# Optimization experiments

Hardware: AMD Instinct MI355X
Metric: run time of the kernel (lower is better)

Reference implementation:

```python
import jax, jax.numpy as jnp
import numpy as np

B, T, D = 2, 1024, 1024
H, HKV = 16, 8
HD = D // H           # 64
NREP = H // HKV       # 2
NLAYERS = 3
MAXKV = T * NLAYERS   # 3072
EPS = 1e-5


def setup_inputs() -> dict:
    key = jax.random.key(0)
    ks = jax.random.split(key, 8)
    # rotary tables over full accumulated-KV range
    inv_freq = 1.0 / (10000.0 ** (jnp.arange(0, HD, 2, dtype=jnp.float32) / HD))  # (HD/2,)
    t = jnp.arange(MAXKV, dtype=jnp.float32)
    freqs = jnp.outer(t, inv_freq)  # (MAXKV, HD/2)
    return {
        "x": jax.random.normal(ks[0], (B, T, D), jnp.float32),
        "cos": jnp.cos(freqs),
        "sin": jnp.sin(freqs),
        "q_w": jax.random.normal(ks[1], (NLAYERS, D, D), jnp.float32) * 0.02,
        "k_w": jax.random.normal(ks[2], (NLAYERS, D // NREP, D), jnp.float32) * 0.02,
        "v_w": jax.random.normal(ks[3], (NLAYERS, D // NREP, D), jnp.float32) * 0.02,
        "ln_w": jnp.ones((NLAYERS, D), jnp.float32),
        "lam": jax.random.normal(ks[4], (NLAYERS,), jnp.float32) * 0.1,
        "out_w": jax.random.normal(ks[5], (D, D), jnp.float32) * 0.02,
        "final_ln_w": jnp.ones((D,), jnp.float32),
        "alpha": jnp.ones((1,), jnp.float32),
    }


def rmsnorm(x, w):
    return x * jax.lax.rsqrt(jnp.mean(x * x, axis=-1, keepdims=True) + EPS) * w


def rope(x, cos, sin):
    # x: (B, L, h, HD); cos/sin: (MAXKV, HD/2); flash_attn non-interleaved rotary
    L = x.shape[1]
    c = jnp.concatenate([cos[:L], cos[:L]], axis=-1)[None, :, None, :]
    s = jnp.concatenate([sin[:L], sin[:L]], axis=-1)[None, :, None, :]
    x1, x2 = jnp.split(x, 2, axis=-1)
    rot = jnp.concatenate([-x2, x1], axis=-1)
    return x * c + rot * s


def reference(x, cos, sin, q_w, k_w, v_w, ln_w, lam, out_w, final_ln_w, alpha):
    scale = HD ** -0.5
    # lambda weights: layernorm over sigmoid of the 3 scalars (biased var, eps=1e-5)
    s = jax.nn.sigmoid(lam)
    lw = (s - s.mean()) * jax.lax.rsqrt(s.var() + EPS)
    qidx = jnp.arange(T)
    k_list, v_list = [], []
    acc = jnp.zeros_like(x)
    for i in range(NLAYERS):
        q = (x @ q_w[i].T).reshape(B, T, H, HD)
        k = (x @ k_w[i].T).reshape(B, T, HKV, HD)
        v = (x @ v_w[i].T).reshape(B, T, HKV, HD)
        k_list.append(k)
        v_list.append(v)
        K = jnp.concatenate(k_list, axis=1)  # (B, L, HKV, HD), L=(i+1)*T
        V = jnp.concatenate(v_list, axis=1)
        L = K.shape[1]
        qr = rope(q, cos, sin)
        Kr = rope(K, cos, sin)  # whole buffer re-rotated each layer, as in original
        Kr = jnp.repeat(Kr, NREP, axis=2)  # GQA expand
        Vr = jnp.repeat(V, NREP, axis=2)
        scores = jnp.einsum('bqhd,bkhd->bhqk', qr, Kr) * scale
        # flash_attn causal=True with kv_len > q_len aligns bottom-right
        mask = jnp.arange(L)[None, :] <= (qidx + (L - T))[:, None]
        scores = jnp.where(mask[None, None], scores, -jnp.inf)
        attn = jax.nn.softmax(scores, axis=-1)
        o = jnp.einsum('bhqk,bkhd->bqhd', attn, Vr).reshape(B, T, D)
        acc = acc + rmsnorm(o, ln_w[i]) * lw[i]
    out = rmsnorm(acc + alpha * x, final_ln_w)
    return out @ out_w.T
```

## Files before the change

kernel.cpp:

```cpp
#include <hip/hip_runtime.h>
#include <type_traits>
#include <utility>

typedef unsigned short u16;
typedef unsigned int u32;
typedef short short8 __attribute__((ext_vector_type(8)));
typedef __bf16 bf16x8 __attribute__((ext_vector_type(8)));
typedef float floatx4 __attribute__((ext_vector_type(4)));

template <typename V, typename = void> struct MfmaTakes : std::false_type {};
template <typename V>
struct MfmaTakes<V, std::void_t<decltype(__builtin_amdgcn_mfma_f32_16x16x32_bf16(
    std::declval<V>(), std::declval<V>(), std::declval<floatx4>(), 0, 0, 0))>>
    : std::true_type {};

template <typename V>
__device__ __forceinline__ floatx4 mfma_impl(V a, V b, floatx4 c, std::true_type) {
  return __builtin_amdgcn_mfma_f32_16x16x32_bf16(a, b, c, 0, 0, 0);
}
template <typename V>
__device__ __forceinline__ floatx4 mfma_impl(V a, V b, floatx4 c, std::false_type) {
  return __builtin_amdgcn_mfma_f32_16x16x32_bf16(
      __builtin_bit_cast(bf16x8, a), __builtin_bit_cast(bf16x8, b), c, 0, 0, 0);
}
__device__ __forceinline__ floatx4 MFMA16(short8 a, short8 b, floatx4 c) {
  return mfma_impl<short8>(a, b, c, MfmaTakes<short8>{});
}

__device__ __forceinline__ u16 f2bf(float f) {
  union { float f; unsigned u; } x; x.f = f;
  unsigned r = (x.u + 0x7fffu + ((x.u >> 16) & 1u)) >> 16;
  return (u16)r;
}
__device__ __forceinline__ float bf2f(u16 v) {
  union { unsigned u; float f; } x; x.u = ((unsigned)v) << 16; return x.f;
}
__device__ __forceinline__ u32 packbf(float lo, float hi) {
  return (__float_as_uint(hi) & 0xffff0000u) | (__float_as_uint(lo) >> 16);
}
__device__ __forceinline__ u32 pack2bf(float lo, float hi) {
  return ((u32)f2bf(hi) << 16) | (u32)f2bf(lo);
}

#if defined(__has_builtin)
#if __has_builtin(__builtin_amdgcn_global_load_lds)
#define HAS_GLLDS 1
#endif
#endif
__device__ __forceinline__ void stage16(const u16* g, u16* lbase, int lane) {
#ifdef HAS_GLLDS
  __builtin_amdgcn_global_load_lds(
      (__attribute__((address_space(1))) void*)(g),
      (__attribute__((address_space(3))) void*)(lbase), 16, 0, 0);
#else
  *(uint4*)(lbase + lane * 8) = *(const uint4*)g;
#endif
}

__global__ __launch_bounds__(256) void prep_kernel(
    const float* __restrict__ x, const float* __restrict__ qw,
    const float* __restrict__ kw, const float* __restrict__ vw,
    const float* __restrict__ outw, const float* __restrict__ lam,
    u16* __restrict__ xb, u16* __restrict__ wcat, u16* __restrict__ outwb,
    float* __restrict__ lwbuf) {
  size_t gid = (size_t)blockIdx.x * 256 + threadIdx.x;
  if (gid == 0) {
    float s0 = 1.f / (1.f + expf(-lam[0]));
    float s1 = 1.f / (1.f + expf(-lam[1]));
    float s2 = 1.f / (1.f + expf(-lam[2]));
    float mean = (s0 + s1 + s2) * (1.f / 3.f);
    float d0 = s0 - mean, d1 = s1 - mean, d2 = s2 - mean;
    float var = (d0 * d0 + d1 * d1 + d2 * d2) * (1.f / 3.f);
    float r = rsqrtf(var + 1e-5f);
    lwbuf[0] = d0 * r; lwbuf[1] = d1 * r; lwbuf[2] = d2 * r;
  }
  if (gid < 524288) {
    float4 v = ((const float4*)x)[gid];
    ushort4 o; o.x = f2bf(v.x); o.y = f2bf(v.y); o.z = f2bf(v.z); o.w = f2bf(v.w);
    ((ushort4*)xb)[gid] = o;
    return;
  }
  size_t g2 = gid - 524288;
  if (g2 < 1572864) {
    int col4 = (int)(g2 & 255);
    int n = (int)(g2 >> 8);
    int layer = n >> 11, r = n & 2047;
    const float* srcrow;
    if (r < 1024) srcrow = qw + ((size_t)(layer * 1024 + r) << 10);
    else if (r < 1536) srcrow = kw + ((size_t)(layer * 512 + (r - 1024)) << 10);
    else srcrow = vw + ((size_t)(layer * 512 + (r - 1536)) << 10);
    float4 v = ((const float4*)srcrow)[col4];
    ushort4 o; o.x = f2bf(v.x); o.y = f2bf(v.y); o.z = f2bf(v.z); o.w = f2bf(v.w);
    ((ushort4*)wcat)[g2] = o;
    return;
  }
  size_t g3 = g2 - 1572864;
  if (g3 < 262144) {
    float4 v = ((const float4*)outw)[g3];
    ushort4 o; o.x = f2bf(v.x); o.y = f2bf(v.y); o.z = f2bf(v.z); o.w = f2bf(v.w);
    ((ushort4*)outwb)[g3] = o;
  }
}

__global__ __launch_bounds__(256) void gemm_qkv(
    const u16* __restrict__ A, const u16* __restrict__ Bw,
    const float* __restrict__ cosb, const float* __restrict__ sinb,
    u16* __restrict__ qr, u16* __restrict__ kr, u16* __restrict__ vt) {
  __shared__ u16 As[128][64];
  __shared__ u16 Bs[128][64];
  const unsigned flat = blockIdx.x;
  const int bm = (flat >> 3) & 15;
  const int bn = ((flat >> 7) << 3) + (flat & 7);
  const int tid = threadIdx.x;
  const int wave = tid >> 6, lane = tid & 63;
  const int quad = lane >> 4, l16 = lane & 15;
  const int wm = wave & 1, wn = wave >> 1;
  const int srow = lane >> 3, skc = (lane & 7) * 8;
  floatx4 acc[4][4];
#pragma unroll
  for (int i = 0; i < 4; i++)
#pragma unroll
    for (int j = 0; j < 4; j++) { acc[i][j][0] = 0.f; acc[i][j][1] = 0.f; acc[i][j][2] = 0.f; acc[i][j][3] = 0.f; }
  const u16* Abase = A + (size_t)(bm * 128) * 1024;
  const u16* Bbase = Bw + (size_t)(bn * 128) * 1024;
  for (int k0 = 0; k0 < 1024; k0 += 64) {
    __syncthreads();
#pragma unroll
    for (int i = 0; i < 4; i++) {
      int ch = wave * 4 + i;
      stage16(Abase + (size_t)(ch * 8 + srow) * 1024 + k0 + skc, &As[ch * 8][0], lane);
      stage16(Bbase + (size_t)(ch * 8 + srow) * 1024 + k0 + skc, &Bs[ch * 8][0], lane);
    }
    __syncthreads();
#pragma unroll
    for (int kf = 0; kf < 2; kf++) {
      short8 af[4], bf[4];
#pragma unroll
      for (int mi = 0; mi < 4; mi++)
        af[mi] = *(const short8*)(&As[wm * 64 + mi * 16 + l16][kf * 32 + quad * 8]);
#pragma unroll
      for (int ni = 0; ni < 4; ni++)
        bf[ni] = *(const short8*)(&Bs[wn * 64 + ni * 16 + l16][kf * 32 + quad * 8]);
#pragma unroll
      for (int mi = 0; mi < 4; mi++)
#pragma unroll
        for (int ni = 0; ni < 4; ni++)
          acc[mi][ni] = MFMA16(af[mi], bf[ni], acc[mi][ni]);
    }
  }
  __syncthreads();
  u16* Tw = (&As[0][0]) + (unsigned)wave * 1056;
  const int f0 = bn * 128 + wn * 64;
  const int lay = f0 >> 11;
  const int r0 = f0 & 2047;
  const int mrow0 = bm * 128 + wm * 64;
  const int jrd = lane & 7, trd = lane >> 3;
  if (r0 < 1536) {
    const bool isQ = (r0 < 1024);
    const int h = isQ ? (r0 >> 6) : ((r0 - 1024) >> 6);
    const float qscale = isQ ? 0.125f : 1.f;
    const int posoff = isQ ? 0 : lay * 1024;
#pragma unroll
    for (int mi = 0; mi < 4; mi++) {
#pragma unroll
      for (int rr = 0; rr < 4; rr++) {
        int m = mrow0 + mi * 16 + quad * 4 + rr;
        int t = m & 1023;
        int pos = posoff + t;
        const float* cp = cosb + (size_t)pos * 32;
        const float* sp = sinb + (size_t)pos * 32;
        float c0 = cp[l16], s0 = sp[l16];
        float c1 = cp[16 + l16], s1 = sp[16 + l16];
        float x10 = acc[mi][0][rr], x20 = acc[mi][2][rr];
        float x11 = acc[mi][1][rr], x21 = acc[mi][3][rr];
        u16* trow = Tw + (quad * 4 + rr) * 66;
        trow[l16]      = f2bf((x10 * c0 - x20 * s0) * qscale);
        trow[16 + l16] = f2bf((x11 * c1 - x21 * s1) * qscale);
        trow[32 + l16] = f2bf((x20 * c0 + x10 * s0) * qscale);
        trow[48 + l16] = f2bf((x21 * c1 + x11 * s1) * qscale);
      }
#pragma unroll
      for (int half = 0; half < 2; half++) {
        int tloc = trd + half * 8;
        uint4 val = *(const uint4*)(Tw + tloc * 66 + jrd * 8);
        int m = mrow0 + mi * 16 + tloc;
        int b = m >> 10, t = m & 1023;
        u16* dst;
        if (isQ) dst = qr + ((((size_t)lay * 2 + b) * 16 + h) * 1024 + t) * 64;
        else     dst = kr + (((size_t)(b * 8 + h)) * 3072 + lay * 1024 + t) * 64;
        *(uint4*)(dst + jrd * 8) = val;
      }
    }
  } else {
    const int hv = (r0 - 1536) >> 6;
    const int b = mrow0 >> 10;
    const int posb = lay * 1024 + (mrow0 & 1023);
#pragma unroll
    for (int ni = 0; ni < 4; ni++) {
#pragma unroll
      for (int mi = 0; mi < 4; mi++) {
        u16* trow = Tw + l16 * 66 + mi * 16 + quad * 4;
        trow[0] = f2bf(acc[mi][ni][0]);
        trow[1] = f2bf(acc[mi][ni][1]);
        trow[2] = f2bf(acc[mi][ni][2]);
        trow[3] = f2bf(acc[mi][ni][3]);
      }
#pragma unroll
      for (int half = 0; half < 2; half++) {
        int dloc = trd + half * 8;
        uint4 val = *(const uint4*)(Tw + dloc * 66 + jrd * 8);
        u16* dst = vt + ((size_t)(b * 8 + hv) * 64 + ni * 16 + dloc) * 3072 + posb + jrd * 8;
        *(uint4*)dst = val;
      }
    }
  }
}

__global__ __launch_bounds__(256) void gemm_bt(
    const u16* __restrict__ A, const u16* __restrict__ Bw,
    float* __restrict__ C, int N, int K) {
  __shared__ u16 As[64][72];
  __shared__ u16 Bs[64][72];
  const int bm = blockIdx.x, bn = blockIdx.y;
  const int tid = threadIdx.x;
  const int wave = tid >> 6, lane = tid & 63;
  const int quad = lane >> 4, l16 = lane & 15;
  const int lr = tid >> 2, lc = (tid & 3) << 4;
  floatx4 acc[4];
#pragma unroll
  for (int i = 0; i < 4; i++) { acc[i][0] = 0.f; acc[i][1] = 0.f; acc[i][2] = 0.f; acc[i][3] = 0.f; }
  const u16* Arow = A + (size_t)(bm * 64 + lr) * K;
  const u16* Brow = Bw + (size_t)(bn * 64 + lr) * K;
  for (int k0 = 0; k0 < K; k0 += 64) {
    __syncthreads();
    *(uint4*)(&As[lr][lc])     = *(const uint4*)(Arow + k0 + lc);
    *(uint4*)(&As[lr][lc + 8]) = *(const uint4*)(Arow + k0 + lc + 8);
    *(uint4*)(&Bs[lr][lc])     = *(const uint4*)(Brow + k0 + lc);
    *(uint4*)(&Bs[lr][lc + 8]) = *(const uint4*)(Brow + k0 + lc + 8);
    __syncthreads();
    const int mrow = wave * 16 + l16;
    short8 a0 = *(const short8*)(&As[mrow][quad * 8]);
    short8 a1 = *(const short8*)(&As[mrow][32 + quad * 8]);
#pragma unroll
    for (int ns = 0; ns < 4; ns++) {
      short8 b0 = *(const short8*)(&Bs[ns * 16 + l16][quad * 8]);
      short8 b1 = *(const short8*)(&Bs[ns * 16 + l16][32 + quad * 8]);
      acc[ns] = MFMA16(a0, b0, acc[ns]);
      acc[ns] = MFMA16(a1, b1, acc[ns]);
    }
  }
#pragma unroll
  for (int ns = 0; ns < 4; ns++)
#pragma unroll
    for (int r = 0; r < 4; r++) {
      int row = bm * 64 + wave * 16 + quad * 4 + r;
      int col = bn * 64 + ns * 16 + l16;
      C[(size_t)row * N + col] = acc[ns][r];
    }
}

__global__ __launch_bounds__(256) void attn_v7(
    const u16* __restrict__ qr, const u16* __restrict__ kr,
    const u16* __restrict__ vt, u16* __restrict__ obS,
    float* __restrict__ lbufp) {
  __shared__ u16 Kt2[2][32][40];
  __shared__ u16 Vtt[64][40];
  const unsigned flat = blockIdx.x;
  const int bhz = (int)((flat & 7) + ((flat >> 5) << 3));
  const int qtile = 3 - (int)((flat >> 3) & 3);
  const int z = bhz >> 5;
  const int bh = bhz & 31;
  const int lay = (z == 5) ? 0 : ((z == 0 || z == 4) ? 1 : 2);
  const int n = lay * 32 + qtile * 8 + 8;
  int kt0, kt1;
  if (lay == 0) { kt0 = 0; kt1 = n; }
  else if (lay == 1) { int hf = n >> 1; kt0 = (z == 0) ? 0 : hf; kt1 = (z == 0) ? hf : n; }
  else {
    int t1 = n / 3, t2 = (2 * n) / 3;
    kt0 = (z == 1) ? 0 : ((z == 2) ? t1 : t2);
    kt1 = (z == 1) ? t1 : ((z == 2) ? t2 : n);
  }
  const int maskkt = lay * 32 + qtile * 8;
  const int b = bh >> 4, h = bh & 15, hk = h >> 1;
  const int tid = threadIdx.x, wave = tid >> 6, lane = tid & 63;
  const int quad = lane >> 4, l16 = lane & 15;
  const int qeffbase = lay * 1024 + qtile * 256 + wave * 64;
  const u16* qpb = qr + ((((size_t)lay * 2 + b) * 16 + h) * 1024
                         + qtile * 256 + wave * 64 + l16) * 64 + quad * 8;
  short8 qf[4][2];
#pragma unroll
  for (int nt = 0; nt < 4; nt++) {
    qf[nt][0] = *(const short8*)(qpb + nt * 1024);
    qf[nt][1] = *(const short8*)(qpb + nt * 1024 + 32);
  }
  const short8 ones = {16256, 16256, 16256, 16256, 16256, 16256, 16256, 16256};
  floatx4 oacc[4][4];
#pragma unroll
  for (int nt = 0; nt < 4; nt++)
#pragma unroll
    for (int dt = 0; dt < 4; dt++) { oacc[nt][dt][0] = 0.f; oacc[nt][dt][1] = 0.f; oacc[nt][dt][2] = 0.f; oacc[nt][dt][3] = 0.f; }
  floatx4 lacc[4];
#pragma unroll
  for (int nt = 0; nt < 4; nt++) { lacc[nt][0] = 0.f; lacc[nt][1] = 0.f; lacc[nt][2] = 0.f; lacc[nt][3] = 0.f; }
  const int ksr = tid >> 3, ksc = (tid & 7) * 8;
  const int ksl = ((ksr >> 3) << 2) + (ksr & 3) + (((ksr >> 2) & 1) << 4);
  u16* kdst = (ksc < 32) ? &Kt2[0][ksl][ksc] : &Kt2[1][ksl][ksc - 32];
  const int vdr = tid >> 2, vdc = (tid & 3) * 8;
  const u16* kp = kr + ((size_t)(b * 8 + hk) * 3072 + kt0 * 32 + ksr) * 64 + ksc;
  const u16* vp = vt + ((size_t)(b * 8 + hk) * 64 + vdr) * 3072 + kt0 * 32 + vdc;
  uint4 kA = *(const uint4*)kp;
  uint4 vA = *(const uint4*)vp;
  for (int kt = kt0; kt < kt1; kt++) {
    kp += 2048; vp += 32;
    __syncthreads();
    *(uint4*)kdst = kA;
    *(uint4*)(&Vtt[vdr][vdc]) = vA;
    if (kt + 1 < kt1) { kA = *(const uint4*)kp; vA = *(const uint4*)vp; }
    __syncthreads();
    const bool needmask = (kt >= maskkt);
    uint2 pk[4][2];
#pragma unroll
    for (int mt = 0; mt < 2; mt++) {
      short8 kfa = *(const short8*)(&Kt2[0][mt * 16 + l16][quad * 8]);
      short8 kfb = *(const short8*)(&Kt2[1][mt * 16 + l16][quad * 8]);
      const int keyb = kt * 32 + quad * 8 + mt * 4;
#pragma unroll
      for (int nt = 0; nt < 4; nt++) {
        floatx4 s; s[0] = 0.f; s[1] = 0.f; s[2] = 0.f; s[3] = 0.f;
        s = MFMA16(kfa, qf[nt][0], s);
        s = MFMA16(kfb, qf[nt][1], s);
        float p0 = __expf(s[0]), p1 = __expf(s[1]);
        float p2 = __expf(s[2]), p3 = __expf(s[3]);
        if (needmask) {
          int qpos = qeffbase + nt * 16 + l16;
          if (keyb + 0 > qpos) p0 = 0.f;
          if (keyb + 1 > qpos) p1 = 0.f;
          if (keyb + 2 > qpos) p2 = 0.f;
          if (keyb + 3 > qpos) p3 = 0.f;
        }
        pk[nt][mt].x = packbf(p0, p1);
        pk[nt][mt].y = packbf(p2, p3);
      }
    }
    short8 vf[4];
#pragma unroll
    for (int dt = 0; dt < 4; dt++)
      vf[dt] = *(const short8*)(&Vtt[dt * 16 + l16][quad * 8]);
#pragma unroll
    for (int nt = 0; nt < 4; nt++) {
      union { uint4 u; short8 s; } pf;
      pf.u.x = pk[nt][0].x; pf.u.y = pk[nt][0].y;
      pf.u.z = pk[nt][1].x; pf.u.w = pk[nt][1].y;
      lacc[nt] = MFMA16(ones, pf.s, lacc[nt]);
#pragma unroll
      for (int dt = 0; dt < 4; dt++)
        oacc[nt][dt] = MFMA16(vf[dt], pf.s, oacc[nt][dt]);
    }
  }
  __syncthreads();
  float* Pf = (float*)(&Kt2[0][0][0]) + (unsigned)wave * 320;
  const int tt = lane >> 2, dd = (lane & 3) << 2;
#pragma unroll
  for (int nt = 0; nt < 4; nt++) {
    int t = qtile * 256 + wave * 64 + nt * 16 + l16;
    if (quad == 0)
      lbufp[((size_t)z * 2048 + b * 1024 + t) * 16 + h] = lacc[nt][0];
    int t2 = qtile * 256 + wave * 64 + nt * 16 + tt;
    u16* orow = obS + ((size_t)(z * 2 + b) * 1024 + t2) * 1024 + h * 64 + dd;
#pragma unroll
    for (int dt = 0; dt < 4; dt++) {
      *(floatx4*)(&Pf[l16 * 20 + quad * 4]) = oacc[nt][dt];
      floatx4 val = *(const floatx4*)(&Pf[tt * 20 + dd]);
      uint2 st; st.x = pack2bf(val[0], val[1]); st.y = pack2bf(val[2], val[3]);
      *(uint2*)(orow + dt * 16) = st;
    }
  }
}

__device__ __forceinline__ float block_sum(float v, float* red) {
  v += __shfl_xor(v, 32); v += __shfl_xor(v, 16); v += __shfl_xor(v, 8);
  v += __shfl_xor(v, 4);  v += __shfl_xor(v, 2);  v += __shfl_xor(v, 1);
  __syncthreads();
  if ((threadIdx.x & 63) == 0) red[threadIdx.x >> 6] = v;
  __syncthreads();
  return red[0] + red[1] + red[2] + red[3];
}

__global__ __launch_bounds__(256) void fused_norm(
    const u16* __restrict__ obS, const float* __restrict__ lbufp,
    const float* __restrict__ x, const float* __restrict__ lnw,
    const float* __restrict__ lwbuf, const float* __restrict__ flnw,
    const float* __restrict__ alphap, u16* __restrict__ y) {
  __shared__ float red[4];
  const int row = blockIdx.x, tid = threadIdx.x;
  float a[4] = {0.f, 0.f, 0.f, 0.f};
  const int nsl[3] = {1, 2, 3};
  const int sl[3][3] = {{5, 0, 0}, {0, 4, 0}, {1, 2, 3}};
#pragma unroll
  for (int l = 0; l < 3; l++) {
    float o0 = 0.f, o1 = 0.f, o2 = 0.f, o3 = 0.f, ls = 0.f;
#pragma unroll
    for (int si = 0; si < 3; si++) {
      if (si >= nsl[l]) break;
      int z = sl[l][si];
      uint2 v = ((const uint2*)(obS + ((size_t)z * 2048 + row) * 1024))[tid];
      o0 += bf2f((u16)(v.x & 0xffff)); o1 += bf2f((u16)(v.x >> 16));
      o2 += bf2f((u16)(v.y & 0xffff)); o3 += bf2f((u16)(v.y >> 16));
      ls += lbufp[((size_t)z * 2048 + row) * 16 + (tid >> 4)];
    }
    float linv = 1.f / ls;
    float v0 = o0 * linv, v1 = o1 * linv, v2 = o2 * linv, v3 = o3 * linv;
    float ss = v0 * v0 + v1 * v1 + v2 * v2 + v3 * v3;
    ss = block_sum(ss, red);
    float rstd = rsqrtf(ss * (1.f / 1024.f) + 1e-5f);
    float lw = lwbuf[l];
    float4 w = ((const float4*)(lnw + (size_t)l * 1024))[tid];
    a[0] += v0 * rstd * w.x * lw;
    a[1] += v1 * rstd * w.y * lw;
    a[2] += v2 * rstd * w.z * lw;
    a[3] += v3 * rstd * w.w * lw;
  }
  const float aa = alphap[0];
  float4 xv = ((const float4*)(x + (size_t)row * 1024))[tid];
  float v0 = a[0] + aa * xv.x, v1 = a[1] + aa * xv.y;
  float v2 = a[2] + aa * xv.z, v3 = a[3] + aa * xv.w;
  float ss = v0 * v0 + v1 * v1 + v2 * v2 + v3 * v3;
  ss = block_sum(ss, red);
  float rstd = rsqrtf(ss * (1.f / 1024.f) + 1e-5f);
  float4 fw = ((const float4*)flnw)[tid];
  ushort4 o;
  o.x = f2bf(v0 * rstd * fw.x); o.y = f2bf(v1 * rstd * fw.y);
  o.z = f2bf(v2 * rstd * fw.z); o.w = f2bf(v3 * rstd * fw.w);
  ((ushort4*)(y + (size_t)row * 1024))[tid] = o;
}

extern "C" void kernel_launch(void* const* d_in, const int* in_sizes, int n_in,
                              void* d_out, int out_size, void* d_ws, size_t ws_size,
                              hipStream_t stream) {
  const float* x     = (const float*)d_in[0];
  const float* cosb  = (const float*)d_in[1];
  const float* sinb  = (const float*)d_in[2];
  const float* qw    = (const float*)d_in[3];
  const float* kw    = (const float*)d_in[4];
  const float* vw    = (const float*)d_in[5];
  const float* lnw   = (const float*)d_in[6];
  const float* lam   = (const float*)d_in[7];
  const float* outw  = (const float*)d_in[8];
  const float* flnw  = (const float*)d_in[9];
  const float* alphap= (const float*)d_in[10];
  float* out = (float*)d_out;
  char* ws = (char*)d_ws;
  u16*   xb    = (u16*)  (ws + 0);
  u16*   wcat  = (u16*)  (ws + 4194304);
  u16*   obS   = (u16*)  (ws + 0);
  u16*   outwb = (u16*)  (ws + 25165824);
  float* lwbuf = (float*)(ws + 27262976);
  u16*   qr    = (u16*)  (ws + 27264000);
  u16*   kr    = (u16*)  (ws + 39846912);
  u16*   vt    = (u16*)  (ws + 46138368);
  float* lbufp = (float*)(ws + 52429824);
  u16*   yb    = (u16*)  (ws + 53216256);

  prep_kernel<<<9216, 256, 0, stream>>>(x, qw, kw, vw, outw, lam, xb, wcat, outwb, lwbuf);
  gemm_qkv<<<768, 256, 0, stream>>>(xb, wcat, cosb, sinb, qr, kr, vt);
  attn_v7<<<768, 256, 0, stream>>>(qr, kr, vt, obS, lbufp);
  fused_norm<<<2048, 256, 0, stream>>>(obS, lbufp, x, lnw, lwbuf, flnw, alphap, yb);
  gemm_bt<<<dim3(32, 16), 256, 0, stream>>>(yb, outwb, out, 1024, 1024);
}
```

Before: 256.1 us.

## Shrink QKV GEMM and attention tiles to raise block count; use exp2 softmax

The QKV projection GEMM moves from 128x128 tiles staged by global_load_lds to 64x64 tiles with padded LDS and plain vector loads, launching 3072 blocks instead of 768. Attention query tiles are halved from 256 to 128 rows, doubling its grid to 1536 blocks. The Q scale is folded with log2(e) so the attention kernel can use exp2f. Smaller tiles are meant to fill all CUs better, at the cost of less operand reuse and more global traffic in the GEMM.

```diff
diff --git a/kernel.cpp b/kernel.cpp
--- a/kernel.cpp
+++ b/kernel.cpp
@@ -40,21 +40,6 @@
 }
 __device__ __forceinline__ u32 pack2bf(float lo, float hi) {
   return ((u32)f2bf(hi) << 16) | (u32)f2bf(lo);
-}
-
-#if defined(__has_builtin)
-#if __has_builtin(__builtin_amdgcn_global_load_lds)
-#define HAS_GLLDS 1
-#endif
-#endif
-__device__ __forceinline__ void stage16(const u16* g, u16* lbase, int lane) {
-#ifdef HAS_GLLDS
-  __builtin_amdgcn_global_load_lds(
-      (__attribute__((address_space(1))) void*)(g),
-      (__attribute__((address_space(3))) void*)(lbase), 16, 0, 0);
-#else
-  *(uint4*)(lbase + lane * 8) = *(const uint4*)g;
-#endif
 }
 
 __global__ __launch_bounds__(256) void prep_kernel(
@@ -102,116 +87,95 @@
   }
 }
 
-__global__ __launch_bounds__(256) void gemm_qkv(
+__global__ __launch_bounds__(256) void gemm_qkv64(
     const u16* __restrict__ A, const u16* __restrict__ Bw,
     const float* __restrict__ cosb, const float* __restrict__ sinb,
     u16* __restrict__ qr, u16* __restrict__ kr, u16* __restrict__ vt) {
-  __shared__ u16 As[128][64];
-  __shared__ u16 Bs[128][64];
-  const unsigned flat = blockIdx.x;
-  const int bm = (flat >> 3) & 15;
-  const int bn = ((flat >> 7) << 3) + (flat & 7);
+  __shared__ u16 As[64][72];
+  __shared__ u16 Bs[64][72];
+  const int bm = blockIdx.x, bn = blockIdx.y;
   const int tid = threadIdx.x;
   const int wave = tid >> 6, lane = tid & 63;
   const int quad = lane >> 4, l16 = lane & 15;
-  const int wm = wave & 1, wn = wave >> 1;
-  const int srow = lane >> 3, skc = (lane & 7) * 8;
-  floatx4 acc[4][4];
-#pragma unroll
-  for (int i = 0; i < 4; i++)
-#pragma unroll
-    for (int j = 0; j < 4; j++) { acc[i][j][0] = 0.f; acc[i][j][1] = 0.f; acc[i][j][2] = 0.f; acc[i][j][3] = 0.f; }
-  const u16* Abase = A + (size_t)(bm * 128) * 1024;
-  const u16* Bbase = Bw + (size_t)(bn * 128) * 1024;
+  const int lr = tid >> 2, lc = (tid & 3) << 4;
+  floatx4 acc[4];
+#pragma unroll
+  for (int i = 0; i < 4; i++) { acc[i][0] = 0.f; acc[i][1] = 0.f; acc[i][2] = 0.f; acc[i][3] = 0.f; }
+  const u16* Arow = A + (size_t)(bm * 64 + lr) * 1024;
+  const u16* Brow = Bw + (size_t)(bn * 64 + lr) * 1024;
   for (int k0 = 0; k0 < 1024; k0 += 64) {
     __syncthreads();
-#pragma unroll
-    for (int i = 0; i < 4; i++) {
-      int ch = wave * 4 + i;
-      stage16(Abase + (size_t)(ch * 8 + srow) * 1024 + k0 + skc, &As[ch * 8][0], lane);
-      stage16(Bbase + (size_t)(ch * 8 + srow) * 1024 + k0 + skc, &Bs[ch * 8][0], lane);
-    }
-    __syncthreads();
-#pragma unroll
-    for (int kf = 0; kf < 2; kf++) {
-      short8 af[4], bf[4];
-#pragma unroll
-      for (int mi = 0; mi < 4; mi++)
-        af[mi] = *(const short8*)(&As[wm * 64 + mi * 16 + l16][kf * 32 + quad * 8]);
-#pragma unroll
-      for (int ni = 0; ni < 4; ni++)
-        bf[ni] = *(const short8*)(&Bs[wn * 64 + ni * 16 + l16][kf * 32 + quad * 8]);
-#pragma unroll
-      for (int mi = 0; mi < 4; mi++)
-#pragma unroll
-        for (int ni = 0; ni < 4; ni++)
-          acc[mi][ni] = MFMA16(af[mi], bf[ni], acc[mi][ni]);
+    *(uint4*)(&As[lr][lc])     = *(const uint4*)(Arow + k0 + lc);
+    *(uint4*)(&As[lr][lc + 8]) = *(const uint4*)(Arow + k0 + lc + 8);
+    *(uint4*)(&Bs[lr][lc])     = *(const uint4*)(Brow + k0 + lc);
+    *(uint4*)(&Bs[lr][lc + 8]) = *(const uint4*)(Brow + k0 + lc + 8);
+    __syncthreads();
+    const int mrow = wave * 16 + l16;
+    short8 a0 = *(const short8*)(&As[mrow][quad * 8]);
+    short8 a1 = *(const short8*)(&As[mrow][32 + quad * 8]);
+#pragma unroll
+    for (int ns = 0; ns < 4; ns++) {
+      short8 b0 = *(const short8*)(&Bs[ns * 16 + l16][quad * 8]);
+      short8 b1 = *(const short8*)(&Bs[ns * 16 + l16][32 + quad * 8]);
+      acc[ns] = MFMA16(a0, b0, acc[ns]);
+      acc[ns] = MFMA16(a1, b1, acc[ns]);
     }
   }
   __syncthreads();
-  u16* Tw = (&As[0][0]) + (unsigned)wave * 1056;
-  const int f0 = bn * 128 + wn * 64;
+  u16* Tw = (&As[0][0]) + (unsigned)wave * 1152;
+  const int f0 = bn * 64;
   const int lay = f0 >> 11;
   const int r0 = f0 & 2047;
-  const int mrow0 = bm * 128 + wm * 64;
+  const int trow_base = bm * 64 + wave * 16;
+  const int b = trow_base >> 10;
   const int jrd = lane & 7, trd = lane >> 3;
   if (r0 < 1536) {
     const bool isQ = (r0 < 1024);
     const int h = isQ ? (r0 >> 6) : ((r0 - 1024) >> 6);
-    const float qscale = isQ ? 0.125f : 1.f;
+    const float qscale = isQ ? 0.18033688f : 1.f;
     const int posoff = isQ ? 0 : lay * 1024;
 #pragma unroll
-    for (int mi = 0; mi < 4; mi++) {
-#pragma unroll
-      for (int rr = 0; rr < 4; rr++) {
-        int m = mrow0 + mi * 16 + quad * 4 + rr;
-        int t = m & 1023;
-        int pos = posoff + t;
-        const float* cp = cosb + (size_t)pos * 32;
-        const float* sp = sinb + (size_t)pos * 32;
-        float c0 = cp[l16], s0 = sp[l16];
-        float c1 = cp[16 + l16], s1 = sp[16 + l16];
-        float x10 = acc[mi][0][rr], x20 = acc[mi][2][rr];
-        float x11 = acc[mi][1][rr], x21 = acc[mi][3][rr];
-        u16* trow = Tw + (quad * 4 + rr) * 66;
-        trow[l16]      = f2bf((x10 * c0 - x20 * s0) * qscale);
-        trow[16 + l16] = f2bf((x11 * c1 - x21 * s1) * qscale);
-        trow[32 + l16] = f2bf((x20 * c0 + x10 * s0) * qscale);
-        trow[48 + l16] = f2bf((x21 * c1 + x11 * s1) * qscale);
-      }
-#pragma unroll
-      for (int half = 0; half < 2; half++) {
-        int tloc = trd + half * 8;
-        uint4 val = *(const uint4*)(Tw + tloc * 66 + jrd * 8);
-        int m = mrow0 + mi * 16 + tloc;
-        int b = m >> 10, t = m & 1023;
-        u16* dst;
-        if (isQ) dst = qr + ((((size_t)lay * 2 + b) * 16 + h) * 1024 + t) * 64;
-        else     dst = kr + (((size_t)(b * 8 + h)) * 3072 + lay * 1024 + t) * 64;
-        *(uint4*)(dst + jrd * 8) = val;
-      }
+    for (int rr = 0; rr < 4; rr++) {
+      int t = (trow_base + quad * 4 + rr) & 1023;
+      int pos = posoff + t;
+      const float* cp = cosb + (size_t)pos * 32;
+      const float* sp = sinb + (size_t)pos * 32;
+      float c0 = cp[l16], s0 = sp[l16];
+      float c1 = cp[16 + l16], s1 = sp[16 + l16];
+      float x10 = acc[0][rr], x20 = acc[2][rr];
+      float x11 = acc[1][rr], x21 = acc[3][rr];
+      u16* trow = Tw + (quad * 4 + rr) * 66;
+      trow[l16]      = f2bf((x10 * c0 - x20 * s0) * qscale);
+      trow[16 + l16] = f2bf((x11 * c1 - x21 * s1) * qscale);
+      trow[32 + l16] = f2bf((x20 * c0 + x10 * s0) * qscale);
+      trow[48 + l16] = f2bf((x21 * c1 + x11 * s1) * qscale);
+    }
+#pragma unroll
+    for (int half = 0; half < 2; half++) {
+      int tloc = trd + half * 8;
+      uint4 val = *(const uint4*)(Tw + tloc * 66 + jrd * 8);
+      int t = (trow_base + tloc) & 1023;
+      u16* dst;
+      if (isQ) dst = qr + ((((size_t)lay * 2 + b) * 16 + h) * 1024 + t) * 64;
+      else     dst = kr + (((size_t)(b * 8 + h)) * 3072 + posoff + t) * 64;
+      *(uint4*)(dst + jrd * 8) = val;
     }
   } else {
     const int hv = (r0 - 1536) >> 6;
-    const int b = mrow0 >> 10;
-    const int posb = lay * 1024 + (mrow0 & 1023);
-#pragma unroll
-    for (int ni = 0; ni < 4; ni++) {
-#pragma unroll
-      for (int mi = 0; mi < 4; mi++) {
-        u16* trow = Tw + l16 * 66 + mi * 16 + quad * 4;
-        trow[0] = f2bf(acc[mi][ni][0]);
-        trow[1] = f2bf(acc[mi][ni][1]);
-        trow[2] = f2bf(acc[mi][ni][2]);
-        trow[3] = f2bf(acc[mi][ni][3]);
-      }
-#pragma unroll
-      for (int half = 0; half < 2; half++) {
-        int dloc = trd + half * 8;
-        uint4 val = *(const uint4*)(Tw + dloc * 66 + jrd * 8);
-        u16* dst = vt + ((size_t)(b * 8 + hv) * 64 + ni * 16 + dloc) * 3072 + posb + jrd * 8;
-        *(uint4*)dst = val;
-      }
+    const int pos0 = lay * 1024 + (trow_base & 1023);
+#pragma unroll
+    for (int ns = 0; ns < 4; ns++) {
+      u16* tr = Tw + (ns * 16 + l16) * 16 + quad * 4;
+      uint2 st;
+      st.x = pack2bf(acc[ns][0], acc[ns][1]);
+      st.y = pack2bf(acc[ns][2], acc[ns][3]);
+      *(uint2*)tr = st;
+    }
+#pragma unroll
+    for (int half = 0; half < 2; half++) {
+      uint4 val = *(const uint4*)(Tw + lane * 16 + half * 8);
+      u16* dst = vt + ((size_t)(b * 8 + hv) * 64 + lane) * 3072 + pos0 + half * 8;
+      *(uint4*)dst = val;
     }
   }
 }
@@ -259,19 +223,19 @@
     }
 }
 
-__global__ __launch_bounds__(256) void attn_v7(
+__global__ __launch_bounds__(256) void attn_v8(
     const u16* __restrict__ qr, const u16* __restrict__ kr,
     const u16* __restrict__ vt, u16* __restrict__ obS,
     float* __restrict__ lbufp) {
   __shared__ u16 Kt2[2][32][40];
   __shared__ u16 Vtt[64][40];
   const unsigned flat = blockIdx.x;
-  const int bhz = (int)((flat & 7) + ((flat >> 5) << 3));
-  const int qtile = 3 - (int)((flat >> 3) & 3);
+  const int bhz = (int)((flat >> 6) * 8 + (flat & 7));
+  const int qtile = 7 - (int)((flat >> 3) & 7);
   const int z = bhz >> 5;
   const int bh = bhz & 31;
   const int lay = (z == 5) ? 0 : ((z == 0 || z == 4) ? 1 : 2);
-  const int n = lay * 32 + qtile * 8 + 8;
+  const int n = lay * 32 + qtile * 4 + 4;
   int kt0, kt1;
   if (lay == 0) { kt0 = 0; kt1 = n; }
   else if (lay == 1) { int hf = n >> 1; kt0 = (z == 0) ? 0 : hf; kt1 = (z == 0) ? hf : n; }
@@ -280,28 +244,28 @@
     kt0 = (z == 1) ? 0 : ((z == 2) ? t1 : t2);
     kt1 = (z == 1) ? t1 : ((z == 2) ? t2 : n);
   }
-  const int maskkt = lay * 32 + qtile * 8;
+  const int maskkt = lay * 32 + qtile * 4;
   const int b = bh >> 4, h = bh & 15, hk = h >> 1;
   const int tid = threadIdx.x, wave = tid >> 6, lane = tid & 63;
   const int quad = lane >> 4, l16 = lane & 15;
-  const int qeffbase = lay * 1024 + qtile * 256 + wave * 64;
+  const int qeffbase = lay * 1024 + qtile * 128 + wave * 32;
   const u16* qpb = qr + ((((size_t)lay * 2 + b) * 16 + h) * 1024
-                         + qtile * 256 + wave * 64 + l16) * 64 + quad * 8;
-  short8 qf[4][2];
-#pragma unroll
-  for (int nt = 0; nt < 4; nt++) {
+                         + qtile * 128 + wave * 32 + l16) * 64 + quad * 8;
+  short8 qf[2][2];
+#pragma unroll
+  for (int nt = 0; nt < 2; nt++) {
     qf[nt][0] = *(const short8*)(qpb + nt * 1024);
     qf[nt][1] = *(const short8*)(qpb + nt * 1024 + 32);
   }
   const short8 ones = {16256, 16256, 16256, 16256, 16256, 16256, 16256, 16256};
-  floatx4 oacc[4][4];
-#pragma unroll
-  for (int nt = 0; nt < 4; nt++)
+  floatx4 oacc[2][4];
+#pragma unroll
+  for (int nt = 0; nt < 2; nt++)
 #pragma unroll
     for (int dt = 0; dt < 4; dt++) { oacc[nt][dt][0] = 0.f; oacc[nt][dt][1] = 0.f; oacc[nt][dt][2] = 0.f; oacc[nt][dt][3] = 0.f; }
-  floatx4 lacc[4];
-#pragma unroll
-  for (int nt = 0; nt < 4; nt++) { lacc[nt][0] = 0.f; lacc[nt][1] = 0.f; lacc[nt][2] = 0.f; lacc[nt][3] = 0.f; }
+  floatx4 lacc[2];
+  lacc[0][0] = 0.f; lacc[0][1] = 0.f; lacc[0][2] = 0.f; lacc[0][3] = 0.f;
+  lacc[1] = lacc[0];
   const int ksr = tid >> 3, ksc = (tid & 7) * 8;
   const int ksl = ((ksr >> 3) << 2) + (ksr & 3) + (((ksr >> 2) & 1) << 4);
   u16* kdst = (ksc < 32) ? &Kt2[0][ksl][ksc] : &Kt2[1][ksl][ksc - 32];
@@ -318,19 +282,19 @@
     if (kt + 1 < kt1) { kA = *(const uint4*)kp; vA = *(const uint4*)vp; }
     __syncthreads();
     const bool needmask = (kt >= maskkt);
-    uint2 pk[4][2];
+    uint2 pk[2][2];
 #pragma unroll
     for (int mt = 0; mt < 2; mt++) {
       short8 kfa = *(const short8*)(&Kt2[0][mt * 16 + l16][quad * 8]);
       short8 kfb = *(const short8*)(&Kt2[1][mt * 16 + l16][quad * 8]);
       const int keyb = kt * 32 + quad * 8 + mt * 4;
 #pragma unroll
-      for (int nt = 0; nt < 4; nt++) {
+      for (int nt = 0; nt < 2; nt++) {
         floatx4 s; s[0] = 0.f; s[1] = 0.f; s[2] = 0.f; s[3] = 0.f;
         s = MFMA16(kfa, qf[nt][0], s);
         s = MFMA16(kfb, qf[nt][1], s);
-        float p0 = __expf(s[0]), p1 = __expf(s[1]);
-        float p2 = __expf(s[2]), p3 = __expf(s[3]);
+        float p0 = exp2f(s[0]), p1 = exp2f(s[1]);
+        float p2 = exp2f(s[2]), p3 = exp2f(s[3]);
         if (needmask) {
           int qpos = qeffbase + nt * 16 + l16;
           if (keyb + 0 > qpos) p0 = 0.f;
@@ -347,7 +311,7 @@
     for (int dt = 0; dt < 4; dt++)
       vf[dt] = *(const short8*)(&Vtt[dt * 16 + l16][quad * 8]);
 #pragma unroll
-    for (int nt = 0; nt < 4; nt++) {
+    for (int nt = 0; nt < 2; nt++) {
       union { uint4 u; short8 s; } pf;
       pf.u.x = pk[nt][0].x; pf.u.y = pk[nt][0].y;
       pf.u.z = pk[nt][1].x; pf.u.w = pk[nt][1].y;
@@ -361,11 +325,11 @@
   float* Pf = (float*)(&Kt2[0][0][0]) + (unsigned)wave * 320;
   const int tt = lane >> 2, dd = (lane & 3) << 2;
 #pragma unroll
-  for (int nt = 0; nt < 4; nt++) {
-    int t = qtile * 256 + wave * 64 + nt * 16 + l16;
+  for (int nt = 0; nt < 2; nt++) {
+    int t = qtile * 128 + wave * 32 + nt * 16 + l16;
     if (quad == 0)
       lbufp[((size_t)z * 2048 + b * 1024 + t) * 16 + h] = lacc[nt][0];
-    int t2 = qtile * 256 + wave * 64 + nt * 16 + tt;
+    int t2 = qtile * 128 + wave * 32 + nt * 16 + tt;
     u16* orow = obS + ((size_t)(z * 2 + b) * 1024 + t2) * 1024 + h * 64 + dd;
 #pragma unroll
     for (int dt = 0; dt < 4; dt++) {
@@ -462,8 +426,8 @@
   u16*   yb    = (u16*)  (ws + 53216256);
 
   prep_kernel<<<9216, 256, 0, stream>>>(x, qw, kw, vw, outw, lam, xb, wcat, outwb, lwbuf);
-  gemm_qkv<<<768, 256, 0, stream>>>(xb, wcat, cosb, sinb, qr, kr, vt);
-  attn_v7<<<768, 256, 0, stream>>>(qr, kr, vt, obS, lbufp);
+  gemm_qkv64<<<dim3(32, 96), 256, 0, stream>>>(xb, wcat, cosb, sinb, qr, kr, vt);
+  attn_v8<<<1536, 256, 0, stream>>>(qr, kr, vt, obS, lbufp);
   fused_norm<<<2048, 256, 0, stream>>>(obS, lbufp, x, lnw, lwbuf, flnw, alphap, yb);
   gemm_bt<<<dim3(32, 16), 256, 0, stream>>>(yb, outwb, out, 1024, 1024);
 }
```

Result: slower. 263.5 us (+2.9%).
